# Kernel tuning notes

Hardware: AMD Instinct MI355X
Metric: run time of the kernel (lower is better)

Reference implementation:

```python
import jax, jax.numpy as jnp
import numpy as np

TAU = 0.07        # temperature from init_kwargs
EPS = 1e-8        # torch F.cosine_similarity eps
NEG_INF = -1e9    # mask fill value used by the original module


def setup_inputs() -> dict:
    key = jax.random.key(0)
    k1, k2 = jax.random.split(key)
    B, D = 4096, 512
    anchor = jax.random.normal(k1, (B, D), dtype=jnp.float32)
    positive = jax.random.normal(k2, (B, D), dtype=jnp.float32)
    return {"anchor": anchor, "positive": positive}


def reference(anchor, positive):
    B = anchor.shape[0]
    N = 2 * B
    emb = jnp.concatenate([anchor, positive], axis=0)          # (2B, D)
    # cosine similarity matrix == normalized dot products (same math as the
    # broadcasted F.cosine_similarity, without the O(N^2 D) intermediate)
    norm = jnp.maximum(jnp.linalg.norm(emb, axis=1, keepdims=True), EPS)
    z = emb / norm
    sim = jnp.matmul(z, z.T) / TAU                             # (2B, 2B)

    idx = jnp.arange(N)
    pos_idx = (idx + B) % N                                    # positive pair index
    pos_logits = sim[idx, pos_idx][:, None]                    # (2B, 1)

    # negatives: everything except self and the positive pair
    neg_mask = (
        jnp.ones((N, N), dtype=bool)
        .at[idx, idx].set(False)
        .at[idx, pos_idx].set(False)
    )
    neg_logits = jnp.where(neg_mask, sim, NEG_INF)             # (2B, 2B)

    all_logits = jnp.concatenate([pos_logits, neg_logits], axis=1)  # (2B, 2B+1)
    loss_per_sample = -pos_logits[:, 0] + jax.scipy.special.logsumexp(all_logits, axis=1)
    # every row has a positive, so valid_samples is all-True; reduction='mean'
    return loss_per_sample.mean()
```

## Files before the change

kernel.cpp:

```cpp
#include <hip/hip_runtime.h>
#include <hip/hip_bf16.h>
#include <stdint.h>


#define N_TOT   8192
#define B_HALF  4096
#define DDIM    512
#define INV_TAU 14.285714285714286f

typedef __bf16 bf16x8 __attribute__((ext_vector_type(8)));
typedef __bf16 bf16x4 __attribute__((ext_vector_type(4)));
typedef float  floatx4 __attribute__((ext_vector_type(4)));

__device__ __forceinline__ void gl2lds16(const void* g, void* l) {
    __builtin_amdgcn_global_load_lds(
        (const __attribute__((address_space(1))) void*)g,
        (__attribute__((address_space(3))) void*)l, 16, 0, 0);
}

__global__ __launch_bounds__(256) void knorm(const float* __restrict__ anchor,
                                             const float* __restrict__ positive,
                                             __bf16* __restrict__ z,
                                             float* __restrict__ row_sums,
                                             float* __restrict__ out) {
    const int row  = blockIdx.x * 4 + (threadIdx.x >> 6);
    const int lane = threadIdx.x & 63;
    if (lane == 0) row_sums[row] = 0.0f;
    if (blockIdx.x == 0 && threadIdx.x == 0) out[0] = 0.0f;
    const float* src = (row < B_HALF) ? (anchor + (size_t)row * DDIM)
                                      : (positive + (size_t)(row - B_HALF) * DDIM);
    float4 v0 = ((const float4*)src)[lane];
    float4 v1 = ((const float4*)src)[lane + 64];
    float ss = v0.x*v0.x + v0.y*v0.y + v0.z*v0.z + v0.w*v0.w
             + v1.x*v1.x + v1.y*v1.y + v1.z*v1.z + v1.w*v1.w;
    #pragma unroll
    for (int m = 1; m < 64; m <<= 1) ss += __shfl_xor(ss, m, 64);
    const float inv = 1.0f / fmaxf(sqrtf(ss), 1e-8f);
    bf16x4 o0, o1;
    o0[0] = (__bf16)(v0.x*inv); o0[1] = (__bf16)(v0.y*inv);
    o0[2] = (__bf16)(v0.z*inv); o0[3] = (__bf16)(v0.w*inv);
    o1[0] = (__bf16)(v1.x*inv); o1[1] = (__bf16)(v1.y*inv);
    o1[2] = (__bf16)(v1.z*inv); o1[3] = (__bf16)(v1.w*inv);
    bf16x4* dst = (bf16x4*)(z + (size_t)row * DDIM);
    dst[lane]      = o0;
    dst[lane + 64] = o1;
}

__global__ __launch_bounds__(1024, 4) void ksim(const __bf16* __restrict__ z,
                                                float* __restrict__ row_sums,
                                                float* __restrict__ pos_sims) {
    const int bid = (int)blockIdx.x;
    const int xcd = bid & 7, l = bid >> 3;
    const int pr  = xcd + 8 * (l / 33);
    const int j   = l % 33;
    int rt, ct;
    if (j <= pr) { rt = j;          ct = pr;      }
    else         { rt = j - pr - 1; ct = 31 - pr; }
    const bool diag = (rt == ct);
    const bool posb = (ct == rt + 16);

    const int r0 = rt * 256, c0 = ct * 256;
    const int tid  = threadIdx.x;
    const int w    = tid >> 6, lane = tid & 63;
    const int quad = lane >> 4, nlo = lane & 15;
    const int wr   = w >> 2,   wc  = w & 3;
    const int wrow = wr * 64,  wcol = wc * 64;

    __shared__ __align__(16) char A0[32768], B0[32768];
    __shared__ __align__(16) char A1[32768], B1[32768];

    floatx4 acc[4][4];
    #pragma unroll
    for (int a = 0; a < 4; a++)
        #pragma unroll
        for (int b = 0; b < 4; b++) acc[a][b] = (floatx4){0.f, 0.f, 0.f, 0.f};

    const int srow = lane >> 3;
    const int p    = lane & 7;

#define STG_A(dst, KB) do {                                                     \
        _Pragma("unroll") for (int it = 0; it < 2; it++) {                      \
            const int c  = w * 2 + it;                                          \
            const int rr = c * 8 + srow;                                        \
            const int lc = (p - rr) & 7;                                        \
            gl2lds16(z + (size_t)(r0 + rr) * DDIM + (KB) + lc * 8,              \
                     (dst) + c * 1024);                                         \
        } } while (0)
#define STG_B(dst, KB) do {                                                     \
        _Pragma("unroll") for (int it = 0; it < 2; it++) {                      \
            const int c  = w * 2 + it;                                          \
            const int rr = c * 8 + srow;                                        \
            const int lc = (p - rr) & 7;                                        \
            gl2lds16(z + (size_t)(c0 + rr) * DDIM + (KB) + lc * 8,              \
                     (dst) + c * 1024);                                         \
        } } while (0)

#define KSTEP(CA, CB, NA, NB, KB_NEXT, DO_STAGE) do {                           \
        if (DO_STAGE) { STG_A(NA, KB_NEXT); if (!diag) STG_B(NB, KB_NEXT); }    \
        const char* Bb_ = diag ? (CA) : (CB);                                   \
        _Pragma("unroll") for (int ks = 0; ks < 2; ks++) {                      \
            bf16x8 af[4], bfr[4];                                               \
            _Pragma("unroll") for (int mi = 0; mi < 4; mi++) {                  \
                const int rr = wrow + mi * 16 + nlo;                            \
                const int pc = (ks * 4 + quad + rr) & 7;                        \
                af[mi] = *(const bf16x8*)((CA) + rr * 128 + pc * 16);           \
            }                                                                   \
            _Pragma("unroll") for (int ni = 0; ni < 4; ni++) {                  \
                const int rr = wcol + ni * 16 + nlo;                            \
                const int pc = (ks * 4 + quad + rr) & 7;                        \
                bfr[ni] = *(const bf16x8*)(Bb_ + rr * 128 + pc * 16);           \
            }                                                                   \
            _Pragma("unroll") for (int mi = 0; mi < 4; mi++)                    \
                _Pragma("unroll") for (int ni = 0; ni < 4; ni++)                \
                    acc[mi][ni] = __builtin_amdgcn_mfma_f32_16x16x32_bf16(      \
                        af[mi], bfr[ni], acc[mi][ni], 0, 0, 0);                 \
        }                                                                       \
        __syncthreads();                                                        \
    } while (0)

    STG_A(A0, 0); if (!diag) STG_B(B0, 0);
    __syncthreads();

    KSTEP(A0, B0, A1, B1,  64, 1);
    KSTEP(A1, B1, A0, B0, 128, 1);
    KSTEP(A0, B0, A1, B1, 192, 1);
    KSTEP(A1, B1, A0, B0, 256, 1);
    KSTEP(A0, B0, A1, B1, 320, 1);
    KSTEP(A1, B1, A0, B0, 384, 1);
    KSTEP(A0, B0, A1, B1, 448, 1);
    KSTEP(A1, B1, A0, B0,   0, 0);

    float* rbuf = (float*)A0;
    float* cbuf = (float*)(A0 + 4096);

    float cs[4] = {0.f, 0.f, 0.f, 0.f};
    #pragma unroll
    for (int mi = 0; mi < 4; mi++) {
        #pragma unroll
        for (int reg = 0; reg < 4; reg++) {
            const int il = wrow + mi * 16 + quad * 4 + reg;
            const int i  = r0 + il;
            const int ipos = i ^ B_HALF;
            float rs = 0.f;
            #pragma unroll
            for (int ni = 0; ni < 4; ni++) {
                const int j2 = c0 + wcol + ni * 16 + nlo;
                const float sim = acc[mi][ni][reg] * INV_TAU;
                float e = __expf(sim - INV_TAU);
                if (diag && j2 == i) e = 0.f;
                if (posb && j2 == ipos) {
                    pos_sims[i]  = sim;
                    pos_sims[j2] = sim;
                }
                rs += e;
                cs[ni] += e;
            }
            rs += __shfl_xor(rs, 1, 64);
            rs += __shfl_xor(rs, 2, 64);
            rs += __shfl_xor(rs, 4, 64);
            rs += __shfl_xor(rs, 8, 64);
            if (nlo == 0) rbuf[il * 4 + wc] = rs;
        }
    }
    if (!diag) {
        #pragma unroll
        for (int ni = 0; ni < 4; ni++) {
            float c = cs[ni];
            c += __shfl_xor(c, 16, 64);
            c += __shfl_xor(c, 32, 64);
            if (quad == 0) cbuf[(wcol + ni * 16 + nlo) * 4 + wr] = c;
        }
    }
    __syncthreads();
    if (tid < 256) {
        const float s = rbuf[tid * 4] + rbuf[tid * 4 + 1]
                      + rbuf[tid * 4 + 2] + rbuf[tid * 4 + 3];
        atomicAdd(&row_sums[r0 + tid], s);
    } else if (tid < 512 && !diag) {
        const int c = tid - 256;
        atomicAdd(&row_sums[c0 + c], cbuf[c * 4] + cbuf[c * 4 + 1]
                                   + cbuf[c * 4 + 2] + cbuf[c * 4 + 3]);
    }
#undef KSTEP
#undef STG_A
#undef STG_B
}

__global__ __launch_bounds__(256) void kfinal(const float* __restrict__ row_sums,
                                              const float* __restrict__ pos_sims,
                                              float* __restrict__ out) {
    const int r = blockIdx.x * 256 + threadIdx.x;
    float v = INV_TAU + __logf(row_sums[r]) - pos_sims[r];
    #pragma unroll
    for (int m = 1; m < 64; m <<= 1) v += __shfl_xor(v, m, 64);
    __shared__ float wsum[4];
    if ((threadIdx.x & 63) == 0) wsum[threadIdx.x >> 6] = v;
    __syncthreads();
    if (threadIdx.x == 0)
        atomicAdd(out, (wsum[0] + wsum[1] + wsum[2] + wsum[3]) * (1.0f / (float)N_TOT));
}

extern "C" void kernel_launch(void* const* d_in, const int* in_sizes, int n_in,
                              void* d_out, int out_size, void* d_ws, size_t ws_size,
                              hipStream_t stream) {
    const float* anchor   = (const float*)d_in[0];
    const float* positive = (const float*)d_in[1];
    float* out = (float*)d_out;

    char* ws = (char*)d_ws;
    __bf16* z        = (__bf16*)ws;
    float*  row_sums = (float*)(ws + 8388608);
    float*  pos_sims = (float*)(ws + 8388608 + 32768);

    knorm<<<N_TOT / 4, 256, 0, stream>>>(anchor, positive, z, row_sums, out);
    ksim<<<528, 1024, 0, stream>>>(z, row_sums, pos_sims);
    kfinal<<<N_TOT / 256, 256, 0, stream>>>(row_sums, pos_sims, out);
}
```

Baseline: 123.5 us.

## Quantize normalized embeddings to FP8 and compute positive sims exactly in fp32

The normalization kernel now writes FP8 (e4m3) embeddings instead of bf16, and the similarity GEMM uses the fp8 MFMA with half as many K-stages, each covering 128 bytes of K. The positive-pair logits are computed in fp32 directly from anchor/positive dot products in the norm kernel, excluded from the GEMM row sums, and added back in the final kernel. This halves the operand bytes and doubles MFMA throughput. In exchange, the negative logits lose precision, which may push the loss past tolerance.

Result: faster. 112.2 us (-9.1%).

```diff
diff --git a/kernel.cpp b/kernel.cpp
--- a/kernel.cpp
+++ b/kernel.cpp
@@ -8,9 +8,7 @@
 #define DDIM    512
 #define INV_TAU 14.285714285714286f
 
-typedef __bf16 bf16x8 __attribute__((ext_vector_type(8)));
-typedef __bf16 bf16x4 __attribute__((ext_vector_type(4)));
-typedef float  floatx4 __attribute__((ext_vector_type(4)));
+typedef float floatx4 __attribute__((ext_vector_type(4)));
 
 __device__ __forceinline__ void gl2lds16(const void* g, void* l) {
     __builtin_amdgcn_global_load_lds(
@@ -20,35 +18,59 @@
 
 __global__ __launch_bounds__(256) void knorm(const float* __restrict__ anchor,
                                              const float* __restrict__ positive,
-                                             __bf16* __restrict__ z,
+                                             uint8_t* __restrict__ z,
                                              float* __restrict__ row_sums,
+                                             float* __restrict__ pos_sims,
                                              float* __restrict__ out) {
-    const int row  = blockIdx.x * 4 + (threadIdx.x >> 6);
+    const int w    = threadIdx.x >> 6;
     const int lane = threadIdx.x & 63;
-    if (lane == 0) row_sums[row] = 0.0f;
+    const int row  = blockIdx.x * 4 + w;
+    const int prow = row + B_HALF;
     if (blockIdx.x == 0 && threadIdx.x == 0) out[0] = 0.0f;
-    const float* src = (row < B_HALF) ? (anchor + (size_t)row * DDIM)
-                                      : (positive + (size_t)(row - B_HALF) * DDIM);
-    float4 v0 = ((const float4*)src)[lane];
-    float4 v1 = ((const float4*)src)[lane + 64];
-    float ss = v0.x*v0.x + v0.y*v0.y + v0.z*v0.z + v0.w*v0.w
-             + v1.x*v1.x + v1.y*v1.y + v1.z*v1.z + v1.w*v1.w;
-    #pragma unroll
-    for (int m = 1; m < 64; m <<= 1) ss += __shfl_xor(ss, m, 64);
-    const float inv = 1.0f / fmaxf(sqrtf(ss), 1e-8f);
-    bf16x4 o0, o1;
-    o0[0] = (__bf16)(v0.x*inv); o0[1] = (__bf16)(v0.y*inv);
-    o0[2] = (__bf16)(v0.z*inv); o0[3] = (__bf16)(v0.w*inv);
-    o1[0] = (__bf16)(v1.x*inv); o1[1] = (__bf16)(v1.y*inv);
-    o1[2] = (__bf16)(v1.z*inv); o1[3] = (__bf16)(v1.w*inv);
-    bf16x4* dst = (bf16x4*)(z + (size_t)row * DDIM);
-    dst[lane]      = o0;
-    dst[lane + 64] = o1;
-}
-
-__global__ __launch_bounds__(1024, 4) void ksim(const __bf16* __restrict__ z,
-                                                float* __restrict__ row_sums,
-                                                float* __restrict__ pos_sims) {
+
+    const float* a = anchor   + (size_t)row * DDIM;
+    const float* p = positive + (size_t)row * DDIM;
+    float4 a0 = ((const float4*)a)[lane];
+    float4 a1 = ((const float4*)a)[lane + 64];
+    float4 p0 = ((const float4*)p)[lane];
+    float4 p1 = ((const float4*)p)[lane + 64];
+
+    float ssa = a0.x*a0.x + a0.y*a0.y + a0.z*a0.z + a0.w*a0.w
+              + a1.x*a1.x + a1.y*a1.y + a1.z*a1.z + a1.w*a1.w;
+    float ssp = p0.x*p0.x + p0.y*p0.y + p0.z*p0.z + p0.w*p0.w
+              + p1.x*p1.x + p1.y*p1.y + p1.z*p1.z + p1.w*p1.w;
+    float dot = a0.x*p0.x + a0.y*p0.y + a0.z*p0.z + a0.w*p0.w
+              + a1.x*p1.x + a1.y*p1.y + a1.z*p1.z + a1.w*p1.w;
+    #pragma unroll
+    for (int m = 1; m < 64; m <<= 1) {
+        ssa += __shfl_xor(ssa, m, 64);
+        ssp += __shfl_xor(ssp, m, 64);
+        dot += __shfl_xor(dot, m, 64);
+    }
+    const float inva = 1.0f / fmaxf(sqrtf(ssa), 1e-8f);
+    const float invp = 1.0f / fmaxf(sqrtf(ssp), 1e-8f);
+    const float psim = dot * inva * invp * INV_TAU;
+    if (lane == 0) {
+        pos_sims[row]  = psim;  pos_sims[prow] = psim;
+        row_sums[row]  = 0.0f;  row_sums[prow] = 0.0f;
+    }
+
+    uint32_t qa0 = __builtin_amdgcn_cvt_pk_fp8_f32(a0.x*inva, a0.y*inva, 0, 0);
+    qa0          = __builtin_amdgcn_cvt_pk_fp8_f32(a0.z*inva, a0.w*inva, qa0, 1);
+    uint32_t qa1 = __builtin_amdgcn_cvt_pk_fp8_f32(a1.x*inva, a1.y*inva, 0, 0);
+    qa1          = __builtin_amdgcn_cvt_pk_fp8_f32(a1.z*inva, a1.w*inva, qa1, 1);
+    uint32_t qp0 = __builtin_amdgcn_cvt_pk_fp8_f32(p0.x*invp, p0.y*invp, 0, 0);
+    qp0          = __builtin_amdgcn_cvt_pk_fp8_f32(p0.z*invp, p0.w*invp, qp0, 1);
+    uint32_t qp1 = __builtin_amdgcn_cvt_pk_fp8_f32(p1.x*invp, p1.y*invp, 0, 0);
+    qp1          = __builtin_amdgcn_cvt_pk_fp8_f32(p1.z*invp, p1.w*invp, qp1, 1);
+    uint32_t* za = (uint32_t*)(z + (size_t)row  * DDIM);
+    uint32_t* zp = (uint32_t*)(z + (size_t)prow * DDIM);
+    za[lane] = qa0; za[lane + 64] = qa1;
+    zp[lane] = qp0; zp[lane + 64] = qp1;
+}
+
+__global__ __launch_bounds__(1024, 4) void ksim(const uint8_t* __restrict__ z,
+                                                float* __restrict__ row_sums) {
     const int bid = (int)blockIdx.x;
     const int xcd = bid & 7, l = bid >> 3;
     const int pr  = xcd + 8 * (l / 33);
@@ -83,7 +105,7 @@
             const int c  = w * 2 + it;                                          \
             const int rr = c * 8 + srow;                                        \
             const int lc = (p - rr) & 7;                                        \
-            gl2lds16(z + (size_t)(r0 + rr) * DDIM + (KB) + lc * 8,              \
+            gl2lds16(z + (size_t)(r0 + rr) * DDIM + (KB) + lc * 16,             \
                      (dst) + c * 1024);                                         \
         } } while (0)
 #define STG_B(dst, KB) do {                                                     \
@@ -91,28 +113,30 @@
             const int c  = w * 2 + it;                                          \
             const int rr = c * 8 + srow;                                        \
             const int lc = (p - rr) & 7;                                        \
-            gl2lds16(z + (size_t)(c0 + rr) * DDIM + (KB) + lc * 8,              \
+            gl2lds16(z + (size_t)(c0 + rr) * DDIM + (KB) + lc * 16,             \
                      (dst) + c * 1024);                                         \
         } } while (0)
 
 #define KSTEP(CA, CB, NA, NB, KB_NEXT, DO_STAGE) do {                           \
         if (DO_STAGE) { STG_A(NA, KB_NEXT); if (!diag) STG_B(NB, KB_NEXT); }    \
         const char* Bb_ = diag ? (CA) : (CB);                                   \
-        _Pragma("unroll") for (int ks = 0; ks < 2; ks++) {                      \
-            bf16x8 af[4], bfr[4];                                               \
+        _Pragma("unroll") for (int ks = 0; ks < 4; ks++) {                      \
+            const int g  = ks * 4 + quad;                \
+            const int lc = g >> 1, h = g & 1;                                   \
+            long af[4], bfr[4];                                                 \
             _Pragma("unroll") for (int mi = 0; mi < 4; mi++) {                  \
                 const int rr = wrow + mi * 16 + nlo;                            \
-                const int pc = (ks * 4 + quad + rr) & 7;                        \
-                af[mi] = *(const bf16x8*)((CA) + rr * 128 + pc * 16);           \
+                const int pc = (lc + rr) & 7;                                   \
+                af[mi] = *(const long*)((CA) + rr * 128 + pc * 16 + h * 8);     \
             }                                                                   \
             _Pragma("unroll") for (int ni = 0; ni < 4; ni++) {                  \
                 const int rr = wcol + ni * 16 + nlo;                            \
-                const int pc = (ks * 4 + quad + rr) & 7;                        \
-                bfr[ni] = *(const bf16x8*)(Bb_ + rr * 128 + pc * 16);           \
+                const int pc = (lc + rr) & 7;                                   \
+                bfr[ni] = *(const long*)(Bb_ + rr * 128 + pc * 16 + h * 8);     \
             }                                                                   \
             _Pragma("unroll") for (int mi = 0; mi < 4; mi++)                    \
                 _Pragma("unroll") for (int ni = 0; ni < 4; ni++)                \
-                    acc[mi][ni] = __builtin_amdgcn_mfma_f32_16x16x32_bf16(      \
+                    acc[mi][ni] = __builtin_amdgcn_mfma_f32_16x16x32_fp8_fp8(   \
                         af[mi], bfr[ni], acc[mi][ni], 0, 0, 0);                 \
         }                                                                       \
         __syncthreads();                                                        \
@@ -121,13 +145,9 @@
     STG_A(A0, 0); if (!diag) STG_B(B0, 0);
     __syncthreads();
 
-    KSTEP(A0, B0, A1, B1,  64, 1);
-    KSTEP(A1, B1, A0, B0, 128, 1);
-    KSTEP(A0, B0, A1, B1, 192, 1);
+    KSTEP(A0, B0, A1, B1, 128, 1);
     KSTEP(A1, B1, A0, B0, 256, 1);
-    KSTEP(A0, B0, A1, B1, 320, 1);
-    KSTEP(A1, B1, A0, B0, 384, 1);
-    KSTEP(A0, B0, A1, B1, 448, 1);
+    KSTEP(A0, B0, A1, B1, 384, 1);
     KSTEP(A1, B1, A0, B0,   0, 0);
 
     float* rbuf = (float*)A0;
@@ -145,13 +165,9 @@
             #pragma unroll
             for (int ni = 0; ni < 4; ni++) {
                 const int j2 = c0 + wcol + ni * 16 + nlo;
-                const float sim = acc[mi][ni][reg] * INV_TAU;
-                float e = __expf(sim - INV_TAU);
+                float e = __expf(acc[mi][ni][reg] * INV_TAU - INV_TAU);
                 if (diag && j2 == i) e = 0.f;
-                if (posb && j2 == ipos) {
-                    pos_sims[i]  = sim;
-                    pos_sims[j2] = sim;
-                }
+                if (posb && j2 == ipos) e = 0.f;
                 rs += e;
                 cs[ni] += e;
             }
@@ -190,7 +206,8 @@
                                               const float* __restrict__ pos_sims,
                                               float* __restrict__ out) {
     const int r = blockIdx.x * 256 + threadIdx.x;
-    float v = INV_TAU + __logf(row_sums[r]) - pos_sims[r];
+    const float ps = pos_sims[r];
+    float v = INV_TAU + __logf(row_sums[r] + __expf(ps - INV_TAU)) - ps;
     #pragma unroll
     for (int m = 1; m < 64; m <<= 1) v += __shfl_xor(v, m, 64);
     __shared__ float wsum[4];
@@ -208,11 +225,12 @@
     float* out = (float*)d_out;
 
     char* ws = (char*)d_ws;
-    __bf16* z        = (__bf16*)ws;
-    float*  row_sums = (float*)(ws + 8388608);
-    float*  pos_sims = (float*)(ws + 8388608 + 32768);
-
-    knorm<<<N_TOT / 4, 256, 0, stream>>>(anchor, positive, z, row_sums, out);
-    ksim<<<528, 1024, 0, stream>>>(z, row_sums, pos_sims);
+    uint8_t* z        = (uint8_t*)ws;
+    float*   row_sums = (float*)(ws + 4194304);
+    float*   pos_sims = (float*)(ws + 4194304 + 32768);
+
+    knorm<<<B_HALF / 4, 256, 0, stream>>>(anchor, positive, z, row_sums,
+                                          pos_sims, out);
+    ksim<<<528, 1024, 0, stream>>>(z, row_sums);
     kfinal<<<N_TOT / 256, 256, 0, stream>>>(row_sums, pos_sims, out);
 }
```
